# Optimization experiments

Measured on AMD Instinct MI355X. Metric: run time of the kernel, lower is better.

## Reference

```python
import jax, jax.numpy as jnp
import numpy as np

E = 16   # n_experts
K = 4    # top_k
NEG = jnp.float32(-1e20)


def _swiglu(x, w1, w2, w3):
    # bias-free SwiGLU expert: (swish(x@w1) * (x@w2)) @ w3
    a = x @ w1
    return (a * jax.nn.sigmoid(a) * (x @ w2)) @ w3


def setup_inputs() -> dict:
    key = jax.random.key(0)
    ks = jax.random.split(key, 9)
    B, S, D, H = 32, 512, 512, 1365  # H = D*2*4//3
    s = 0.02  # weight init scale to keep activations sane
    return {
        "x": jax.random.normal(ks[0], (B, S, D), jnp.float32),
        "gate_w": jax.random.normal(ks[1], (D, E), jnp.float32) * s,
        "routing_bias": jnp.zeros((E,), jnp.float32),
        "w1": jax.random.normal(ks[2], (E, D, H), jnp.float32) * s,
        "w2": jax.random.normal(ks[3], (E, D, H), jnp.float32) * s,
        "w3": jax.random.normal(ks[4], (E, H, D), jnp.float32) * s,
        "sw1": jax.random.normal(ks[5], (D, H), jnp.float32) * s,
        "sw2": jax.random.normal(ks[6], (D, H), jnp.float32) * s,
        "sw3": jax.random.normal(ks[7], (H, D), jnp.float32) * s,
    }


def reference(x, gate_w, routing_bias, w1, w2, w3, sw1, sw2, sw3):
    # gate logits + aux-free load-balancing bias  [B,S,E]
    gate_out = x @ gate_w + routing_bias
    top_v, top_i = jax.lax.top_k(gate_out, K)
    # chosen[b,s,e] = 1 if expert e is in the top-k for token (b,s)
    chosen = jax.nn.one_hot(top_i, E, dtype=x.dtype).sum(axis=-2)
    # scatter top-k values onto a -1e20 background, then softmax over experts
    masked = jnp.where(chosen > 0, gate_out, NEG)
    probs = jax.nn.softmax(masked, axis=-1)
    weights = probs * chosen  # zero outside the chosen set (matches torch mask)
    # shared expert runs on all tokens
    out = _swiglu(x, sw1, sw2, sw3)
    # per-expert SwiGLU, weighted-combined (loop over fixed small E)
    for e in range(E):
        out = out + _swiglu(x, w1[e], w2[e], w3[e]) * weights[..., e:e + 1]
    return out
```

## Files before the change

### kernel.cpp

```cpp
#include <hip/hip_runtime.h>

#define NT    16384
#define DDIM  512
#define HDIM  1365
#define HPAD  1408
#define NEXP  16
#define BK    64
#define BM    128
#define MAXTILES 656
#define MAXSLOTS 83968

typedef unsigned short u16;
typedef unsigned int   u32;
typedef __attribute__((ext_vector_type(8))) __bf16 bf16x8;
typedef __attribute__((ext_vector_type(4))) float  f32x4;
typedef __attribute__((address_space(3))) void lds_void;
typedef __attribute__((address_space(1))) void glb_void;

__device__ __forceinline__ u16 f2bf(float f) {
  union { float f; u32 u; } v; v.f = f;
  u32 u = v.u;
  u += 0x7fffu + ((u >> 16) & 1u);
  return (u16)(u >> 16);
}

__device__ __forceinline__ float bf2f(u16 b) {
  union { u32 u; float f; } v; v.u = ((u32)b) << 16;
  return v.f;
}

__device__ __forceinline__ f32x4 mfma16(bf16x8 a, bf16x8 b, f32x4 c) {
  return __builtin_amdgcn_mfma_f32_16x16x32_bf16(a, b, c, 0, 0, 0);
}

__device__ __forceinline__ void gload16(const u16* g, u16* l) {
  __builtin_amdgcn_global_load_lds((const glb_void*)g, (lds_void*)l, 16, 0, 0);
}

__device__ __forceinline__ bf16x8 lds_frag(const u16* base, int row, int e0) {
  int b = ((row << 7) + (e0 << 1)) ^ ((row & 7) << 4);
  return *(const bf16x8*)((const char*)base + b);
}

__device__ __forceinline__ int swz_n(int bid, int n) {
  int q = n >> 3, r = n & 7;
  int xcd = bid & 7, j = bid >> 3;
  return (xcd < r ? xcd * (q + 1) : r * (q + 1) + (xcd - r) * q) + j;
}

__global__ void transpose12_kernel(const float* __restrict__ w1, const float* __restrict__ w2,
                                   const float* __restrict__ sw1, const float* __restrict__ sw2,
                                   u16* __restrict__ w1t, u16* __restrict__ w2t,
                                   u16* __restrict__ sw1t, u16* __restrict__ sw2t) {
  __shared__ float tile[32][65];
  int z = blockIdx.z;
  const float* in; u16* out;
  if (z < 16)      { in = w1 + (size_t)z * DDIM * HDIM;        out = w1t + (size_t)z * HPAD * DDIM; }
  else if (z < 32) { in = w2 + (size_t)(z - 16) * DDIM * HDIM; out = w2t + (size_t)(z - 16) * HPAD * DDIM; }
  else if (z == 32){ in = sw1; out = sw1t; }
  else             { in = sw2; out = sw2t; }
  int h0 = blockIdx.x * 32, d0 = blockIdx.y * 64;
  int tx = threadIdx.x, ty = threadIdx.y;
  int h = h0 + tx;
#pragma unroll
  for (int r = 0; r < 8; ++r) {
    int d = d0 + ty + r * 8;
    float v = (h < HDIM) ? in[(size_t)d * HDIM + h] : 0.f;
    tile[tx][ty + r * 8] = v;
  }
  __syncthreads();
#pragma unroll
  for (int r = 0; r < 4; ++r) {
    int hh = h0 + ty + r * 8;
    u32 lo = f2bf(tile[ty + r * 8][2 * tx]);
    u32 hi = f2bf(tile[ty + r * 8][2 * tx + 1]);
    ((u32*)&out[(size_t)hh * DDIM + d0])[tx] = lo | (hi << 16);
  }
}

__global__ void transpose3_kernel(const float* __restrict__ w3, const float* __restrict__ sw3,
                                  u16* __restrict__ w3t, u16* __restrict__ sw3t) {
  __shared__ float tile[32][65];
  int z = blockIdx.z;
  const float* in = (z < 16) ? (w3 + (size_t)z * HDIM * DDIM) : sw3;
  u16* out = (z < 16) ? (w3t + (size_t)z * DDIM * HPAD) : sw3t;
  int h0 = blockIdx.x * 64, d0 = blockIdx.y * 32;
  int tx = threadIdx.x, ty = threadIdx.y;
  int d = d0 + tx;
#pragma unroll
  for (int r = 0; r < 8; ++r) {
    int h = h0 + ty + r * 8;
    float v = (h < HDIM) ? in[(size_t)h * DDIM + d] : 0.f;
    tile[tx][ty + r * 8] = v;
  }
  __syncthreads();
#pragma unroll
  for (int r = 0; r < 4; ++r) {
    int dd = d0 + ty + r * 8;
    u32 lo = f2bf(tile[ty + r * 8][2 * tx]);
    u32 hi = f2bf(tile[ty + r * 8][2 * tx + 1]);
    ((u32*)&out[(size_t)dd * HPAD + h0])[tx] = lo | (hi << 16);
  }
}

__global__ __launch_bounds__(512) void routing_kernel(
    const float* __restrict__ x, const float* __restrict__ gw,
    const float* __restrict__ rbias, u16* __restrict__ x_bf,
    int* __restrict__ top_e, float* __restrict__ top_w) {
  __shared__ float gwp[NEXP * DDIM];
  int tid = threadIdx.x;
  for (int i = tid; i < NEXP * DDIM; i += 512) {
    int d = i >> 4, e = i & 15;
    gwp[e * DDIM + ((d & 7) << 6) + (d >> 3)] = gw[i];
  }
  __syncthreads();
  int w = tid >> 6, lane = tid & 63;
  int t = blockIdx.x * 8 + w;
  const float* xr = x + (size_t)t * DDIM + lane * 8;
  float4 xa = ((const float4*)xr)[0], xb = ((const float4*)xr)[1];
  float xv[8] = {xa.x, xa.y, xa.z, xa.w, xb.x, xb.y, xb.z, xb.w};
  u16 r[8];
#pragma unroll
  for (int k = 0; k < 8; ++k) r[k] = f2bf(xv[k]);
  *(uint4*)&x_bf[(size_t)t * DDIM + lane * 8] = *(const uint4*)r;
  float acc[NEXP];
#pragma unroll
  for (int e = 0; e < NEXP; ++e) {
    const float* ge = gwp + e * DDIM + lane;
    float s = 0.f;
#pragma unroll
    for (int k = 0; k < 8; ++k) s += xv[k] * ge[k << 6];
#pragma unroll
    for (int off = 32; off; off >>= 1) s += __shfl_xor(s, off);
    acc[e] = s + rbias[e];
  }
  if (lane == 0) {
    int sel[4]; float sv[4];
    unsigned used = 0;
#pragma unroll
    for (int i = 0; i < 4; ++i) {
      float best = -1e30f; int bi = 0;
#pragma unroll
      for (int e = 0; e < NEXP; ++e) {
        bool ok = !((used >> e) & 1u) && acc[e] > best;
        best = ok ? acc[e] : best;
        bi   = ok ? e : bi;
      }
      used |= 1u << bi; sel[i] = bi; sv[i] = best;
    }
    float m = sv[0];
    float ex[4]; float s = 0.f;
#pragma unroll
    for (int i = 0; i < 4; ++i) { ex[i] = __expf(sv[i] - m); s += ex[i]; }
    float inv = 1.f / s;
#pragma unroll
    for (int i = 0; i < 4; ++i) {
      top_e[t * 4 + i] = sel[i];
      top_w[t * 4 + i] = ex[i] * inv;
    }
  }
}

__global__ __launch_bounds__(1024) void rank_kernel(const int* __restrict__ top_e,
                                                    int* __restrict__ counts,
                                                    int* __restrict__ top_pos) {
  __shared__ int hist[NEXP], base[NEXP];
  int tid = threadIdx.x;
  int t = blockIdx.x * 1024 + tid;
  if (tid < NEXP) hist[tid] = 0;
  __syncthreads();
  int e4[4], r4[4];
#pragma unroll
  for (int i = 0; i < 4; ++i) {
    e4[i] = top_e[t * 4 + i];
    r4[i] = atomicAdd(&hist[e4[i]], 1);
  }
  __syncthreads();
  if (tid < NEXP) base[tid] = atomicAdd(&counts[tid], hist[tid]);
  __syncthreads();
#pragma unroll
  for (int i = 0; i < 4; ++i) top_pos[t * 4 + i] = base[e4[i]] + r4[i];
}

__global__ __launch_bounds__(256) void finish_kernel(
    const int* __restrict__ counts, const int* __restrict__ top_e,
    const float* __restrict__ top_w, const int* __restrict__ top_pos,
    int* __restrict__ slot_off, int* __restrict__ ntiles, int2* __restrict__ desc,
    int* __restrict__ tok_pad, float* __restrict__ w_pad, int* __restrict__ pos_list) {
  __shared__ int s_off[17], s_tb[17], s_nt[17], s_cnt[17];
  int tid = threadIdx.x;
  if (tid == 0) {
    int off = 0, td = 0;
    for (int e = 0; e < 17; ++e) {
      int c = (e == 16) ? NT : counts[e];
      s_cnt[e] = c; s_off[e] = off;
      int nt = (c + BM - 1) / BM;
      s_nt[e] = nt; s_tb[e] = td;
      td += nt; off += nt * BM;
    }
    if (blockIdx.x == 0) {
      for (int e = 0; e < 17; ++e) slot_off[e] = s_off[e];
      slot_off[17] = off;
      *ntiles = td;
    }
  }
  __syncthreads();
  if (blockIdx.x == 0) {
    for (int e = 0; e < 17; ++e)
      for (int i = tid; i < s_nt[e]; i += 256)
        desc[s_tb[e] + i] = make_int2(e, s_off[e] + i * BM);
  } else if (blockIdx.x == 1) {
    for (int e = 0; e < 16; ++e) {
      int c = s_cnt[e], padded = s_nt[e] * BM;
      for (int i = c + tid; i < padded; i += 256) {
        tok_pad[s_off[e] + i] = 0;
        w_pad[s_off[e] + i] = 0.f;
      }
    }
  }
  int t = blockIdx.x * 256 + tid;
#pragma unroll
  for (int i = 0; i < 4; ++i) {
    int e = top_e[t * 4 + i];
    int slot = s_off[e] + top_pos[t * 4 + i];
    tok_pad[slot] = t;
    w_pad[slot] = top_w[t * 4 + i];
    pos_list[t * 4 + i] = slot;
  }
  int sh = s_off[16] + t;
  tok_pad[sh] = t;
  w_pad[sh] = 1.f;
}

__global__ __launch_bounds__(256, 3) void gemm1_kernel(
    const u16* __restrict__ x_bf, const u16* __restrict__ w1t, const u16* __restrict__ w2t,
    const u16* __restrict__ sw1t, const u16* __restrict__ sw2t,
    const int* __restrict__ ntiles, const int2* __restrict__ desc,
    const int* __restrict__ tok_pad, u16* __restrict__ h, int lo, int ntc) {
  int wk = swz_n(blockIdx.x, ntc * 22);
  int tloc = wk / 22, hblk = wk - tloc * 22;
  int ti = (lo >> 7) + tloc;
  if (ti >= *ntiles) return;
  int2 de = desc[ti];
  int e = de.x, m0 = de.y;
  int n0 = hblk * 64;
  const u16* W1 = (e == 16) ? sw1t : (w1t + (size_t)e * HPAD * DDIM);
  const u16* W2 = (e == 16) ? sw2t : (w2t + (size_t)e * HPAD * DDIM);

  __shared__ u16 smem[16384];
  u16* xs = smem;
  u16* bs = smem + 8192;

  int tid = threadIdx.x, w = tid >> 6, lane = tid & 63;
  int wm = w >> 1, wn = w & 1, lr = lane & 15, lk = lane >> 4;

  const u16* ags[4]; const u16* bgs[4];
  int ce = (((lane & 7) ^ ((lane >> 3) & 7)) << 3);
#pragma unroll
  for (int p = 0; p < 4; ++p) {
    int r = w * 32 + p * 8 + (lane >> 3);
    ags[p] = x_bf + (size_t)tok_pad[m0 + r] * DDIM + ce;
    int grp = (w * 32 + p * 8) >> 4;
    const u16* Wsrc = (grp & 1) ? W2 : W1;
    int hrow = n0 + ((grp >> 1) << 4) + (r & 15);
    bgs[p] = Wsrc + (size_t)hrow * DDIM + ce;
  }

  f32x4 acc[4][4] = {};

  for (int ks = 0; ks < DDIM / BK; ++ks) {
    int k0 = ks * BK;
#pragma unroll
    for (int p = 0; p < 4; ++p) {
      gload16(ags[p] + k0, xs + ((w * 32 + p * 8) << 6));
      gload16(bgs[p] + k0, bs + ((w * 32 + p * 8) << 6));
    }
    __syncthreads();
#pragma unroll
    for (int kf = 0; kf < 2; ++kf) {
      int e0 = kf * 32 + lk * 8;
      bf16x8 bfr[4];
#pragma unroll
      for (int nf = 0; nf < 4; ++nf)
        bfr[nf] = lds_frag(bs, wn * 64 + nf * 16 + lr, e0);
#pragma unroll
      for (int mf = 0; mf < 4; ++mf) {
        bf16x8 a = lds_frag(xs, wm * 64 + mf * 16 + lr, e0);
#pragma unroll
        for (int nf = 0; nf < 4; ++nf)
          acc[mf][nf] = mfma16(a, bfr[nf], acc[mf][nf]);
      }
    }
    __syncthreads();
  }

  u16* hs = smem;
#pragma unroll
  for (int mf = 0; mf < 4; ++mf)
#pragma unroll
    for (int nf = 0; nf < 4; nf += 2)
#pragma unroll
      for (int j = 0; j < 4; ++j) {
        float g = acc[mf][nf][j], u = acc[mf][nf + 1][j];
        float hv = g * u / (1.f + __expf(-g));
        int row = wm * 64 + mf * 16 + lk * 4 + j;
        int col = wn * 32 + (nf >> 1) * 16 + lr;
        hs[((row << 6) + col) ^ ((row & 7) << 3)] = f2bf(hv);
      }
  __syncthreads();
#pragma unroll
  for (int i = 0; i < 4; ++i) {
    int idx = (i * 256 + tid) * 8;
    int row = idx >> 6, col = idx & 63;
    *(uint4*)&h[(size_t)(m0 - lo + row) * HPAD + n0 + col] =
        *(uint4*)&hs[idx ^ ((row & 7) << 3)];
  }
}

template <bool YMODE>
__global__ __launch_bounds__(256, 3) void gemm2_kernel(
    const u16* __restrict__ h, const u16* __restrict__ w3t, const u16* __restrict__ sw3t,
    const int* __restrict__ ntiles, const int2* __restrict__ desc,
    const int* __restrict__ tok_pad, const float* __restrict__ w_pad,
    u16* __restrict__ y, float* __restrict__ out, int lo, int ntc) {
  int wk = swz_n(blockIdx.x, ntc * 4);
  int tloc = wk >> 2, dblk = wk & 3;
  int ti = (lo >> 7) + tloc;
  if (ti >= *ntiles) return;
  int2 de = desc[ti];
  int e = de.x, m0 = de.y;
  int n0 = dblk * 128;
  const u16* W3 = (e == 16) ? sw3t : (w3t + (size_t)e * DDIM * HPAD);

  __shared__ u16 smem[16384];
  __shared__ float swl[BM];
  u16* hs = smem;
  u16* ws3 = smem + 8192;

  int tid = threadIdx.x, w = tid >> 6, lane = tid & 63;
  int wm = w >> 1, wn = w & 1, lr = lane & 15, lk = lane >> 4;

  if (tid < BM) swl[tid] = w_pad[m0 + tid];

  const u16* ags[4]; const u16* bgs[4];
  int ce = (((lane & 7) ^ ((lane >> 3) & 7)) << 3);
#pragma unroll
  for (int p = 0; p < 4; ++p) {
    int r = w * 32 + p * 8 + (lane >> 3);
    ags[p] = h + (size_t)(m0 - lo + r) * HPAD + ce;
    bgs[p] = W3 + (size_t)(n0 + r) * HPAD + ce;
  }

  f32x4 acc[4][4] = {};

  for (int ks = 0; ks < HPAD / BK; ++ks) {
    int k0 = ks * BK;
#pragma unroll
    for (int p = 0; p < 4; ++p) {
      gload16(ags[p] + k0, hs + ((w * 32 + p * 8) << 6));
      gload16(bgs[p] + k0, ws3 + ((w * 32 + p * 8) << 6));
    }
    __syncthreads();
#pragma unroll
    for (int kf = 0; kf < 2; ++kf) {
      int e0 = kf * 32 + lk * 8;
      bf16x8 bfr[4];
#pragma unroll
      for (int nf = 0; nf < 4; ++nf)
        bfr[nf] = lds_frag(ws3, wn * 64 + nf * 16 + lr, e0);
#pragma unroll
      for (int mf = 0; mf < 4; ++mf) {
        bf16x8 a = lds_frag(hs, wm * 64 + mf * 16 + lr, e0);
#pragma unroll
        for (int nf = 0; nf < 4; ++nf)
          acc[mf][nf] = mfma16(a, bfr[nf], acc[mf][nf]);
      }
    }
    __syncthreads();
  }

  if constexpr (YMODE) {
    u16* ys = smem;
#pragma unroll
    for (int mf = 0; mf < 4; ++mf)
#pragma unroll
      for (int j = 0; j < 4; ++j) {
        int row = wm * 64 + mf * 16 + lk * 4 + j;
        float wv = swl[row];
#pragma unroll
        for (int nf = 0; nf < 4; ++nf)
          ys[((row << 7) + wn * 64 + nf * 16 + lr) ^ ((row & 7) << 3)] =
              f2bf(acc[mf][nf][j] * wv);
      }
    __syncthreads();
#pragma unroll
    for (int i = 0; i < 8; ++i) {
      int idx = (i * 256 + tid) * 8;
      int row = idx >> 7, col = idx & 127;
      *(uint4*)&y[(size_t)(m0 + row) * DDIM + n0 + col] =
          *(uint4*)&smem[idx ^ ((row & 7) << 3)];
    }
  } else {
#pragma unroll
    for (int mf = 0; mf < 4; ++mf)
#pragma unroll
      for (int j = 0; j < 4; ++j) {
        int row = wm * 64 + mf * 16 + lk * 4 + j;
        float wv = swl[row];
        float* orow = out + (size_t)tok_pad[m0 + row] * DDIM + n0;
#pragma unroll
        for (int nf = 0; nf < 4; ++nf)
          atomicAdd(&orow[wn * 64 + nf * 16 + lr], acc[mf][nf][j] * wv);
      }
  }
}

__global__ void reduce_kernel(const u16* __restrict__ y, const int* __restrict__ pos_list,
                              const int* __restrict__ slot_off, float* __restrict__ out) {
  int t = blockIdx.x;
  int c = threadIdx.x;
  int4 pl = ((const int4*)pos_list)[t];
  int sh = slot_off[16] + t;
  ushort4 a = ((const ushort4*)(y + (size_t)sh * DDIM))[c];
  ushort4 b = ((const ushort4*)(y + (size_t)pl.x * DDIM))[c];
  ushort4 d = ((const ushort4*)(y + (size_t)pl.y * DDIM))[c];
  ushort4 e = ((const ushort4*)(y + (size_t)pl.z * DDIM))[c];
  ushort4 f = ((const ushort4*)(y + (size_t)pl.w * DDIM))[c];
  float4 s;
  s.x = bf2f(a.x) + bf2f(b.x) + bf2f(d.x) + bf2f(e.x) + bf2f(f.x);
  s.y = bf2f(a.y) + bf2f(b.y) + bf2f(d.y) + bf2f(e.y) + bf2f(f.y);
  s.z = bf2f(a.z) + bf2f(b.z) + bf2f(d.z) + bf2f(e.z) + bf2f(f.z);
  s.w = bf2f(a.w) + bf2f(b.w) + bf2f(d.w) + bf2f(e.w) + bf2f(f.w);
  ((float4*)(out + (size_t)t * DDIM))[c] = s;
}

extern "C" void kernel_launch(void* const* d_in, const int* in_sizes, int n_in,
                              void* d_out, int out_size, void* d_ws, size_t ws_size,
                              hipStream_t stream) {
  const float* x      = (const float*)d_in[0];
  const float* gate_w = (const float*)d_in[1];
  const float* rbias  = (const float*)d_in[2];
  const float* w1     = (const float*)d_in[3];
  const float* w2     = (const float*)d_in[4];
  const float* w3     = (const float*)d_in[5];
  const float* sw1    = (const float*)d_in[6];
  const float* sw2    = (const float*)d_in[7];
  const float* sw3    = (const float*)d_in[8];
  float* out = (float*)d_out;

  char* ws = (char*)d_ws;
  size_t off = 0;
  auto alloc = [&](size_t bytes) -> char* {
    char* p = ws + off;
    off += (bytes + 255) & ~(size_t)255;
    return p;
  };
  u16* x_bf  = (u16*)alloc((size_t)NT * DDIM * 2);
  u16* w1t   = (u16*)alloc((size_t)NEXP * HPAD * DDIM * 2);
  u16* w2t   = (u16*)alloc((size_t)NEXP * HPAD * DDIM * 2);
  u16* w3t   = (u16*)alloc((size_t)NEXP * DDIM * HPAD * 2);
  u16* sw1t  = (u16*)alloc((size_t)HPAD * DDIM * 2);
  u16* sw2t  = (u16*)alloc((size_t)HPAD * DDIM * 2);
  u16* sw3t  = (u16*)alloc((size_t)DDIM * HPAD * 2);
  int*   counts   = (int*)alloc(64 * 4);
  int*   top_e    = (int*)alloc((size_t)NT * 4 * 4);
  float* top_w    = (float*)alloc((size_t)NT * 4 * 4);
  int*   top_pos  = (int*)alloc((size_t)NT * 4 * 4);
  int*   slot_off = (int*)alloc(32 * 4);
  int*   ntiles   = (int*)alloc(256);
  int2*  desc     = (int2*)alloc((size_t)MAXTILES * 8);
  int*   tok_pad  = (int*)alloc((size_t)MAXSLOTS * 4);
  float* w_pad    = (float*)alloc((size_t)MAXSLOTS * 4);
  int*   pos_list = (int*)alloc((size_t)NT * 4 * 4);
  size_t y_off = off;
  u16* y = (u16*)alloc((size_t)MAXSLOTS * DDIM * 2);
  size_t h_off_y = off;
  (void)in_sizes; (void)n_in; (void)ws_size;

  const size_t per_row = (size_t)HPAD * 2;
  bool ymode;
  size_t h_off, rows_avail;
  size_t avail_y = (ws_size > h_off_y) ? (ws_size - h_off_y) : 0;
  if (avail_y / per_row >= 10496) {
    ymode = true; h_off = h_off_y; rows_avail = avail_y / per_row;
  } else {
    ymode = false; h_off = y_off;
    size_t avail_a = (ws_size > y_off) ? (ws_size - y_off) : 0;
    rows_avail = avail_a / per_row;
  }
  int CS;
  if (rows_avail >= (size_t)MAXSLOTS) CS = MAXSLOTS;
  else {
    CS = (int)((rows_avail / 2048) * 2048);
    if (CS < 2048) CS = (int)((rows_avail / BM) * BM);
    if (CS < BM) CS = BM;
  }
  int NCH = (MAXSLOTS + CS - 1) / CS;
  u16* h = (u16*)(ws + h_off);

  hipMemsetAsync(counts, 0, 64 * 4, stream);
  if (!ymode) hipMemsetAsync(out, 0, (size_t)out_size * 4, stream);

  dim3 tb(32, 8);
  transpose12_kernel<<<dim3(HPAD / 32, DDIM / 64, 34), tb, 0, stream>>>(
      w1, w2, sw1, sw2, w1t, w2t, sw1t, sw2t);
  transpose3_kernel<<<dim3(HPAD / 64, DDIM / 32, 17), tb, 0, stream>>>(
      w3, sw3, w3t, sw3t);

  routing_kernel<<<NT / 8, 512, 0, stream>>>(x, gate_w, rbias, x_bf, top_e, top_w);
  rank_kernel<<<NT / 1024, 1024, 0, stream>>>(top_e, counts, top_pos);
  finish_kernel<<<NT / 256, 256, 0, stream>>>(counts, top_e, top_w, top_pos,
                                              slot_off, ntiles, desc,
                                              tok_pad, w_pad, pos_list);

  for (int c = 0; c < NCH; ++c) {
    int lo = c * CS;
    int ntc = (MAXSLOTS - lo < CS ? MAXSLOTS - lo : CS) >> 7;
    gemm1_kernel<<<ntc * 22, 256, 0, stream>>>(
        x_bf, w1t, w2t, sw1t, sw2t, ntiles, desc, tok_pad, h, lo, ntc);
    if (ymode)
      gemm2_kernel<true><<<ntc * 4, 256, 0, stream>>>(
          h, w3t, sw3t, ntiles, desc, tok_pad, w_pad, y, out, lo, ntc);
    else
      gemm2_kernel<false><<<ntc * 4, 256, 0, stream>>>(
          h, w3t, sw3t, ntiles, desc, tok_pad, w_pad, y, out, lo, ntc);
  }
  if (ymode) reduce_kernel<<<NT, 128, 0, stream>>>(y, pos_list, slot_off, out);
}
```

Measured before the change: 587.0 us.

## Widen GEMM tiles to 128x256 with 512-thread blocks in both expert GEMMs

Both grouped GEMMs move from 256-thread blocks with 128x128 output tiles to 512-thread blocks with 128x256 tiles, arranged as 8 waves in a 2x4 grid. Each block now loads the A operand (token rows or h rows) once for twice as many output columns, which cuts redundant A traffic and halves the block count. The epilogues are reorganized to match, with the gemm2 Y-mode store split into two halves that reuse the shared-memory staging buffer. In exchange, LDS use per block rises, occupancy is capped at 2 blocks per CU, and there are fewer blocks to fill the GPU.

Result: slower. 709.4 us (+20.9%).

```diff
diff --git a/kernel.cpp b/kernel.cpp
--- a/kernel.cpp
+++ b/kernel.cpp
@@ -232,37 +232,42 @@
   w_pad[sh] = 1.f;
 }
 
-__global__ __launch_bounds__(256, 3) void gemm1_kernel(
+__global__ __launch_bounds__(512, 2) void gemm1_kernel(
     const u16* __restrict__ x_bf, const u16* __restrict__ w1t, const u16* __restrict__ w2t,
     const u16* __restrict__ sw1t, const u16* __restrict__ sw2t,
     const int* __restrict__ ntiles, const int2* __restrict__ desc,
     const int* __restrict__ tok_pad, u16* __restrict__ h, int lo, int ntc) {
-  int wk = swz_n(blockIdx.x, ntc * 22);
-  int tloc = wk / 22, hblk = wk - tloc * 22;
+  int wk = swz_n(blockIdx.x, ntc * 11);
+  int tloc = wk / 11, hblk = wk - tloc * 11;
   int ti = (lo >> 7) + tloc;
   if (ti >= *ntiles) return;
   int2 de = desc[ti];
   int e = de.x, m0 = de.y;
-  int n0 = hblk * 64;
+  int n0 = hblk * 128;
   const u16* W1 = (e == 16) ? sw1t : (w1t + (size_t)e * HPAD * DDIM);
   const u16* W2 = (e == 16) ? sw2t : (w2t + (size_t)e * HPAD * DDIM);
 
-  __shared__ u16 smem[16384];
+  __shared__ u16 smem[24576];
   u16* xs = smem;
   u16* bs = smem + 8192;
 
   int tid = threadIdx.x, w = tid >> 6, lane = tid & 63;
-  int wm = w >> 1, wn = w & 1, lr = lane & 15, lk = lane >> 4;
-
-  const u16* ags[4]; const u16* bgs[4];
-  int ce = (((lane & 7) ^ ((lane >> 3) & 7)) << 3);
+  int wm = w >> 2, wn = w & 3, lr = lane & 15, lk = lane >> 4;
+
+  const u16* ags[2]; const u16* bgs[4];
+#pragma unroll
+  for (int p = 0; p < 2; ++p) {
+    int r = p * 64 + w * 8 + (lane >> 3);
+    int ce = (((lane & 7) ^ (r & 7)) << 3);
+    ags[p] = x_bf + (size_t)tok_pad[m0 + r] * DDIM + ce;
+  }
 #pragma unroll
   for (int p = 0; p < 4; ++p) {
-    int r = w * 32 + p * 8 + (lane >> 3);
-    ags[p] = x_bf + (size_t)tok_pad[m0 + r] * DDIM + ce;
-    int grp = (w * 32 + p * 8) >> 4;
+    int rb = p * 64 + w * 8 + (lane >> 3);
+    int ce = (((lane & 7) ^ (rb & 7)) << 3);
+    int grp = (p * 64 + w * 8) >> 4;
     const u16* Wsrc = (grp & 1) ? W2 : W1;
-    int hrow = n0 + ((grp >> 1) << 4) + (r & 15);
+    int hrow = n0 + ((grp >> 1) << 4) + (rb & 15);
     bgs[p] = Wsrc + (size_t)hrow * DDIM + ce;
   }
 
@@ -271,10 +276,11 @@
   for (int ks = 0; ks < DDIM / BK; ++ks) {
     int k0 = ks * BK;
 #pragma unroll
-    for (int p = 0; p < 4; ++p) {
-      gload16(ags[p] + k0, xs + ((w * 32 + p * 8) << 6));
-      gload16(bgs[p] + k0, bs + ((w * 32 + p * 8) << 6));
-    }
+    for (int p = 0; p < 2; ++p)
+      gload16(ags[p] + k0, xs + ((p * 64 + w * 8) << 6));
+#pragma unroll
+    for (int p = 0; p < 4; ++p)
+      gload16(bgs[p] + k0, bs + ((p * 64 + w * 8) << 6));
     __syncthreads();
 #pragma unroll
     for (int kf = 0; kf < 2; ++kf) {
@@ -298,57 +304,62 @@
 #pragma unroll
   for (int mf = 0; mf < 4; ++mf)
 #pragma unroll
-    for (int nf = 0; nf < 4; nf += 2)
+    for (int hc = 0; hc < 2; ++hc)
 #pragma unroll
       for (int j = 0; j < 4; ++j) {
-        float g = acc[mf][nf][j], u = acc[mf][nf + 1][j];
+        float g = acc[mf][hc * 2][j], u = acc[mf][hc * 2 + 1][j];
         float hv = g * u / (1.f + __expf(-g));
         int row = wm * 64 + mf * 16 + lk * 4 + j;
-        int col = wn * 32 + (nf >> 1) * 16 + lr;
-        hs[((row << 6) + col) ^ ((row & 7) << 3)] = f2bf(hv);
+        int col = (wn * 2 + hc) * 16 + lr;
+        hs[((row << 7) + col) ^ ((row & 7) << 3)] = f2bf(hv);
       }
   __syncthreads();
 #pragma unroll
   for (int i = 0; i < 4; ++i) {
-    int idx = (i * 256 + tid) * 8;
-    int row = idx >> 6, col = idx & 63;
+    int idx = (i * 512 + tid) * 8;
+    int row = idx >> 7, col = idx & 127;
     *(uint4*)&h[(size_t)(m0 - lo + row) * HPAD + n0 + col] =
         *(uint4*)&hs[idx ^ ((row & 7) << 3)];
   }
 }
 
 template <bool YMODE>
-__global__ __launch_bounds__(256, 3) void gemm2_kernel(
+__global__ __launch_bounds__(512, 2) void gemm2_kernel(
     const u16* __restrict__ h, const u16* __restrict__ w3t, const u16* __restrict__ sw3t,
     const int* __restrict__ ntiles, const int2* __restrict__ desc,
     const int* __restrict__ tok_pad, const float* __restrict__ w_pad,
     u16* __restrict__ y, float* __restrict__ out, int lo, int ntc) {
-  int wk = swz_n(blockIdx.x, ntc * 4);
-  int tloc = wk >> 2, dblk = wk & 3;
+  int wk = swz_n(blockIdx.x, ntc * 2);
+  int tloc = wk >> 1, dblk = wk & 1;
   int ti = (lo >> 7) + tloc;
   if (ti >= *ntiles) return;
   int2 de = desc[ti];
   int e = de.x, m0 = de.y;
-  int n0 = dblk * 128;
+  int n0 = dblk * 256;
   const u16* W3 = (e == 16) ? sw3t : (w3t + (size_t)e * DDIM * HPAD);
 
-  __shared__ u16 smem[16384];
+  __shared__ u16 smem[24576];
   __shared__ float swl[BM];
   u16* hs = smem;
   u16* ws3 = smem + 8192;
 
   int tid = threadIdx.x, w = tid >> 6, lane = tid & 63;
-  int wm = w >> 1, wn = w & 1, lr = lane & 15, lk = lane >> 4;
+  int wm = w >> 2, wn = w & 3, lr = lane & 15, lk = lane >> 4;
 
   if (tid < BM) swl[tid] = w_pad[m0 + tid];
 
-  const u16* ags[4]; const u16* bgs[4];
-  int ce = (((lane & 7) ^ ((lane >> 3) & 7)) << 3);
+  const u16* ags[2]; const u16* bgs[4];
+#pragma unroll
+  for (int p = 0; p < 2; ++p) {
+    int r = p * 64 + w * 8 + (lane >> 3);
+    int ce = (((lane & 7) ^ (r & 7)) << 3);
+    ags[p] = h + (size_t)(m0 - lo + r) * HPAD + ce;
+  }
 #pragma unroll
   for (int p = 0; p < 4; ++p) {
-    int r = w * 32 + p * 8 + (lane >> 3);
-    ags[p] = h + (size_t)(m0 - lo + r) * HPAD + ce;
-    bgs[p] = W3 + (size_t)(n0 + r) * HPAD + ce;
+    int rb = p * 64 + w * 8 + (lane >> 3);
+    int ce = (((lane & 7) ^ (rb & 7)) << 3);
+    bgs[p] = W3 + (size_t)(n0 + rb) * HPAD + ce;
   }
 
   f32x4 acc[4][4] = {};
@@ -356,10 +367,11 @@
   for (int ks = 0; ks < HPAD / BK; ++ks) {
     int k0 = ks * BK;
 #pragma unroll
-    for (int p = 0; p < 4; ++p) {
-      gload16(ags[p] + k0, hs + ((w * 32 + p * 8) << 6));
-      gload16(bgs[p] + k0, ws3 + ((w * 32 + p * 8) << 6));
-    }
+    for (int p = 0; p < 2; ++p)
+      gload16(ags[p] + k0, hs + ((p * 64 + w * 8) << 6));
+#pragma unroll
+    for (int p = 0; p < 4; ++p)
+      gload16(bgs[p] + k0, ws3 + ((p * 64 + w * 8) << 6));
     __syncthreads();
 #pragma unroll
     for (int kf = 0; kf < 2; ++kf) {
@@ -382,23 +394,31 @@
   if constexpr (YMODE) {
     u16* ys = smem;
 #pragma unroll
-    for (int mf = 0; mf < 4; ++mf)
-#pragma unroll
-      for (int j = 0; j < 4; ++j) {
-        int row = wm * 64 + mf * 16 + lk * 4 + j;
-        float wv = swl[row];
-#pragma unroll
-        for (int nf = 0; nf < 4; ++nf)
-          ys[((row << 7) + wn * 64 + nf * 16 + lr) ^ ((row & 7) << 3)] =
-              f2bf(acc[mf][nf][j] * wv);
-      }
-    __syncthreads();
-#pragma unroll
-    for (int i = 0; i < 8; ++i) {
-      int idx = (i * 256 + tid) * 8;
-      int row = idx >> 7, col = idx & 127;
-      *(uint4*)&y[(size_t)(m0 + row) * DDIM + n0 + col] =
-          *(uint4*)&smem[idx ^ ((row & 7) << 3)];
+    for (int half = 0; half < 2; ++half) {
+      if ((wn >> 1) == half) {
+        int wnl = wn & 1;
+#pragma unroll
+        for (int mf = 0; mf < 4; ++mf)
+#pragma unroll
+          for (int j = 0; j < 4; ++j) {
+            int row = wm * 64 + mf * 16 + lk * 4 + j;
+            float wv = swl[row];
+#pragma unroll
+            for (int nf = 0; nf < 4; ++nf) {
+              int col = wnl * 64 + nf * 16 + lr;
+              ys[((row << 7) + col) ^ ((row & 7) << 3)] = f2bf(acc[mf][nf][j] * wv);
+            }
+          }
+      }
+      __syncthreads();
+#pragma unroll
+      for (int i = 0; i < 4; ++i) {
+        int idx = (i * 512 + tid) * 8;
+        int row = idx >> 7, col = idx & 127;
+        *(uint4*)&y[(size_t)(m0 + row) * DDIM + n0 + half * 128 + col] =
+            *(uint4*)&ys[idx ^ ((row & 7) << 3)];
+      }
+      __syncthreads();
     }
   } else {
 #pragma unroll
@@ -516,13 +536,13 @@
   for (int c = 0; c < NCH; ++c) {
     int lo = c * CS;
     int ntc = (MAXSLOTS - lo < CS ? MAXSLOTS - lo : CS) >> 7;
-    gemm1_kernel<<<ntc * 22, 256, 0, stream>>>(
+    gemm1_kernel<<<ntc * 11, 512, 0, stream>>>(
         x_bf, w1t, w2t, sw1t, sw2t, ntiles, desc, tok_pad, h, lo, ntc);
     if (ymode)
-      gemm2_kernel<true><<<ntc * 4, 256, 0, stream>>>(
+      gemm2_kernel<true><<<ntc * 2, 512, 0, stream>>>(
           h, w3t, sw3t, ntiles, desc, tok_pad, w_pad, y, out, lo, ntc);
     else
-      gemm2_kernel<false><<<ntc * 4, 256, 0, stream>>>(
+      gemm2_kernel<false><<<ntc * 2, 512, 0, stream>>>(
           h, w3t, sw3t, ntiles, desc, tok_pad, w_pad, y, out, lo, ntc);
   }
   if (ymode) reduce_kernel<<<NT, 128, 0, stream>>>(y, pos_list, slot_off, out);
```

## Enlarge gemm1 tile to 256x128 with 512 threads and double-buffered LDS

Applied to the files above, without the earlier changes.

Expert padding granularity grows from 128 to 256 rows. gemm1 now uses 512-thread blocks computing a 256-row by 128-column (gate+up) tile. The K loop is double-buffered with waitcnt and barriers so global loads overlap the MFMA work. gemm2 keeps its 128-row tiles by splitting each 256-row tile into two sub-tiles. The goal is more operand reuse per LDS load and hidden load latency, at the cost of more padding waste, 128KB of LDS, and lower occupancy.

Result: slower. 666.1 us (+13.5%).

```diff
diff --git a/kernel.cpp b/kernel.cpp
--- a/kernel.cpp
+++ b/kernel.cpp
@@ -6,9 +6,8 @@
 #define HPAD  1408
 #define NEXP  16
 #define BK    64
-#define BM    128
-#define MAXTILES 656
-#define MAXSLOTS 83968
+#define MAXTILES 336
+#define MAXSLOTS 86016
 
 typedef unsigned short u16;
 typedef unsigned int   u32;
@@ -194,9 +193,9 @@
     for (int e = 0; e < 17; ++e) {
       int c = (e == 16) ? NT : counts[e];
       s_cnt[e] = c; s_off[e] = off;
-      int nt = (c + BM - 1) / BM;
+      int nt = (c + 255) >> 8;
       s_nt[e] = nt; s_tb[e] = td;
-      td += nt; off += nt * BM;
+      td += nt; off += nt * 256;
     }
     if (blockIdx.x == 0) {
       for (int e = 0; e < 17; ++e) slot_off[e] = s_off[e];
@@ -208,10 +207,10 @@
   if (blockIdx.x == 0) {
     for (int e = 0; e < 17; ++e)
       for (int i = tid; i < s_nt[e]; i += 256)
-        desc[s_tb[e] + i] = make_int2(e, s_off[e] + i * BM);
+        desc[s_tb[e] + i] = make_int2(e, s_off[e] + i * 256);
   } else if (blockIdx.x == 1) {
     for (int e = 0; e < 16; ++e) {
-      int c = s_cnt[e], padded = s_nt[e] * BM;
+      int c = s_cnt[e], padded = s_nt[e] * 256;
       for (int i = c + tid; i < padded; i += 256) {
         tok_pad[s_off[e] + i] = 0;
         w_pad[s_off[e] + i] = 0.f;
@@ -232,87 +231,103 @@
   w_pad[sh] = 1.f;
 }
 
-__global__ __launch_bounds__(256, 3) void gemm1_kernel(
+__global__ __launch_bounds__(512, 2) void gemm1_kernel(
     const u16* __restrict__ x_bf, const u16* __restrict__ w1t, const u16* __restrict__ w2t,
     const u16* __restrict__ sw1t, const u16* __restrict__ sw2t,
     const int* __restrict__ ntiles, const int2* __restrict__ desc,
     const int* __restrict__ tok_pad, u16* __restrict__ h, int lo, int ntc) {
-  int wk = swz_n(blockIdx.x, ntc * 22);
-  int tloc = wk / 22, hblk = wk - tloc * 22;
-  int ti = (lo >> 7) + tloc;
+  int wk = swz_n(blockIdx.x, ntc * 11);
+  int tloc = wk / 11, hblk = wk - tloc * 11;
+  int ti = (lo >> 8) + tloc;
   if (ti >= *ntiles) return;
   int2 de = desc[ti];
   int e = de.x, m0 = de.y;
-  int n0 = hblk * 64;
+  int n0h = hblk * 128;
   const u16* W1 = (e == 16) ? sw1t : (w1t + (size_t)e * HPAD * DDIM);
   const u16* W2 = (e == 16) ? sw2t : (w2t + (size_t)e * HPAD * DDIM);
 
-  __shared__ u16 smem[16384];
-  u16* xs = smem;
-  u16* bs = smem + 8192;
+  __shared__ u16 smem[65536];
+  u16* As = smem;
+  u16* Bs = smem + 32768;
 
   int tid = threadIdx.x, w = tid >> 6, lane = tid & 63;
-  int wm = w >> 1, wn = w & 1, lr = lane & 15, lk = lane >> 4;
+  int wm = w >> 2, wn = w & 3, lr = lane & 15, lk = lane >> 4;
 
   const u16* ags[4]; const u16* bgs[4];
-  int ce = (((lane & 7) ^ ((lane >> 3) & 7)) << 3);
-#pragma unroll
-  for (int p = 0; p < 4; ++p) {
-    int r = w * 32 + p * 8 + (lane >> 3);
-    ags[p] = x_bf + (size_t)tok_pad[m0 + r] * DDIM + ce;
-    int grp = (w * 32 + p * 8) >> 4;
+#pragma unroll
+  for (int l = 0; l < 4; ++l) {
+    int idx = l * 512 + tid;
+    int row = idx >> 3, sl = idx & 7;
+    int ce = ((sl ^ (row & 7)) << 3);
+    ags[l] = x_bf + (size_t)tok_pad[m0 + row] * DDIM + ce;
+    int grp = row >> 4;
     const u16* Wsrc = (grp & 1) ? W2 : W1;
-    int hrow = n0 + ((grp >> 1) << 4) + (r & 15);
-    bgs[p] = Wsrc + (size_t)hrow * DDIM + ce;
-  }
-
-  f32x4 acc[4][4] = {};
-
-  for (int ks = 0; ks < DDIM / BK; ++ks) {
-    int k0 = ks * BK;
-#pragma unroll
-    for (int p = 0; p < 4; ++p) {
-      gload16(ags[p] + k0, xs + ((w * 32 + p * 8) << 6));
-      gload16(bgs[p] + k0, bs + ((w * 32 + p * 8) << 6));
-    }
-    __syncthreads();
+    int hrow = n0h + ((grp >> 1) << 4) + (row & 15);
+    bgs[l] = Wsrc + (size_t)hrow * DDIM + ce;
+  }
+
+  auto stage = [&](int kt, int buf) {
+    int k0 = kt * BK;
+#pragma unroll
+    for (int l = 0; l < 4; ++l) {
+      int db = buf * 16384 + l * 4096 + (w << 9);
+      gload16(ags[l] + k0, As + db);
+      gload16(bgs[l] + k0, Bs + db);
+    }
+  };
+
+  f32x4 acc[8][4] = {};
+
+  stage(0, 0);
+  stage(1, 1);
+
+  for (int t = 0; t < DDIM / BK; ++t) {
+    int cur = t & 1;
+    asm volatile("s_waitcnt vmcnt(8)" ::: "memory");
+    __builtin_amdgcn_s_barrier();
+    const u16* Ab = As + cur * 16384;
+    const u16* Bb = Bs + cur * 16384;
 #pragma unroll
     for (int kf = 0; kf < 2; ++kf) {
       int e0 = kf * 32 + lk * 8;
       bf16x8 bfr[4];
 #pragma unroll
       for (int nf = 0; nf < 4; ++nf)
-        bfr[nf] = lds_frag(bs, wn * 64 + nf * 16 + lr, e0);
-#pragma unroll
-      for (int mf = 0; mf < 4; ++mf) {
-        bf16x8 a = lds_frag(xs, wm * 64 + mf * 16 + lr, e0);
+        bfr[nf] = lds_frag(Bb, wn * 64 + nf * 16 + lr, e0);
+#pragma unroll
+      for (int mf = 0; mf < 8; ++mf) {
+        bf16x8 a = lds_frag(Ab, wm * 128 + mf * 16 + lr, e0);
 #pragma unroll
         for (int nf = 0; nf < 4; ++nf)
           acc[mf][nf] = mfma16(a, bfr[nf], acc[mf][nf]);
       }
     }
-    __syncthreads();
-  }
+    __builtin_amdgcn_s_barrier();
+    int tn = (t + 2 < DDIM / BK) ? t + 2 : DDIM / BK - 1;
+    stage(tn, cur);
+  }
+  asm volatile("s_waitcnt vmcnt(0)" ::: "memory");
+  __builtin_amdgcn_s_barrier();
 
   u16* hs = smem;
 #pragma unroll
-  for (int mf = 0; mf < 4; ++mf)
-#pragma unroll
-    for (int nf = 0; nf < 4; nf += 2)
+  for (int mf = 0; mf < 8; ++mf)
+#pragma unroll
+    for (int hc = 0; hc < 2; ++hc)
 #pragma unroll
       for (int j = 0; j < 4; ++j) {
-        float g = acc[mf][nf][j], u = acc[mf][nf + 1][j];
+        float g = acc[mf][hc * 2][j], u = acc[mf][hc * 2 + 1][j];
         float hv = g * u / (1.f + __expf(-g));
-        int row = wm * 64 + mf * 16 + lk * 4 + j;
-        int col = wn * 32 + (nf >> 1) * 16 + lr;
-        hs[((row << 6) + col) ^ ((row & 7) << 3)] = f2bf(hv);
-      }
-  __syncthreads();
-#pragma unroll
-  for (int i = 0; i < 4; ++i) {
-    int idx = (i * 256 + tid) * 8;
-    int row = idx >> 6, col = idx & 63;
-    *(uint4*)&h[(size_t)(m0 - lo + row) * HPAD + n0 + col] =
+        int row = wm * 128 + mf * 16 + lk * 4 + j;
+        int col = (wn * 2 + hc) * 16 + lr;
+        hs[((row << 7) + col) ^ ((row & 7) << 3)] = f2bf(hv);
+      }
+  __syncthreads();
+#pragma unroll
+  for (int i = 0; i < 8; ++i) {
+    int idx = (i * 512 + tid) * 8;
+    int row = idx >> 7, col = idx & 127;
+    *(uint4*)&h[(size_t)(m0 - lo + row) * HPAD + n0h + col] =
         *(uint4*)&hs[idx ^ ((row & 7) << 3)];
   }
 }
@@ -323,24 +338,24 @@
     const int* __restrict__ ntiles, const int2* __restrict__ desc,
     const int* __restrict__ tok_pad, const float* __restrict__ w_pad,
     u16* __restrict__ y, float* __restrict__ out, int lo, int ntc) {
-  int wk = swz_n(blockIdx.x, ntc * 4);
-  int tloc = wk >> 2, dblk = wk & 3;
-  int ti = (lo >> 7) + tloc;
+  int wk = swz_n(blockIdx.x, ntc * 8);
+  int tloc = wk >> 3, sub = (wk >> 2) & 1, dblk = wk & 3;
+  int ti = (lo >> 8) + tloc;
   if (ti >= *ntiles) return;
   int2 de = desc[ti];
-  int e = de.x, m0 = de.y;
+  int e = de.x, m0 = de.y + sub * 128;
   int n0 = dblk * 128;
   const u16* W3 = (e == 16) ? sw3t : (w3t + (size_t)e * DDIM * HPAD);
 
   __shared__ u16 smem[16384];
-  __shared__ float swl[BM];
+  __shared__ float swl[128];
   u16* hs = smem;
   u16* ws3 = smem + 8192;
 
   int tid = threadIdx.x, w = tid >> 6, lane = tid & 63;
   int wm = w >> 1, wn = w & 1, lr = lane & 15, lk = lane >> 4;
 
-  if (tid < BM) swl[tid] = w_pad[m0 + tid];
+  if (tid < 128) swl[tid] = w_pad[m0 + tid];
 
   const u16* ags[4]; const u16* bgs[4];
   int ce = (((lane & 7) ^ ((lane >> 3) & 7)) << 3);
@@ -481,7 +496,7 @@
   bool ymode;
   size_t h_off, rows_avail;
   size_t avail_y = (ws_size > h_off_y) ? (ws_size - h_off_y) : 0;
-  if (avail_y / per_row >= 10496) {
+  if (avail_y / per_row >= 10752) {
     ymode = true; h_off = h_off_y; rows_avail = avail_y / per_row;
   } else {
     ymode = false; h_off = y_off;
@@ -492,8 +507,8 @@
   if (rows_avail >= (size_t)MAXSLOTS) CS = MAXSLOTS;
   else {
     CS = (int)((rows_avail / 2048) * 2048);
-    if (CS < 2048) CS = (int)((rows_avail / BM) * BM);
-    if (CS < BM) CS = BM;
+    if (CS < 2048) CS = (int)((rows_avail / 256) * 256);
+    if (CS < 256) CS = 256;
   }
   int NCH = (MAXSLOTS + CS - 1) / CS;
   u16* h = (u16*)(ws + h_off);
@@ -515,14 +530,14 @@
 
   for (int c = 0; c < NCH; ++c) {
     int lo = c * CS;
-    int ntc = (MAXSLOTS - lo < CS ? MAXSLOTS - lo : CS) >> 7;
-    gemm1_kernel<<<ntc * 22, 256, 0, stream>>>(
+    int ntc = (MAXSLOTS - lo < CS ? MAXSLOTS - lo : CS) >> 8;
+    gemm1_kernel<<<ntc * 11, 512, 0, stream>>>(
         x_bf, w1t, w2t, sw1t, sw2t, ntiles, desc, tok_pad, h, lo, ntc);
     if (ymode)
-      gemm2_kernel<true><<<ntc * 4, 256, 0, stream>>>(
+      gemm2_kernel<true><<<ntc * 8, 256, 0, stream>>>(
           h, w3t, sw3t, ntiles, desc, tok_pad, w_pad, y, out, lo, ntc);
     else
-      gemm2_kernel<false><<<ntc * 4, 256, 0, stream>>>(
+      gemm2_kernel<false><<<ntc * 8, 256, 0, stream>>>(
           h, w3t, sw3t, ntiles, desc, tok_pad, w_pad, y, out, lo, ntc);
   }
   if (ymode) reduce_kernel<<<NT, 128, 0, stream>>>(y, pos_list, slot_off, out);
```
